# Kernel tuning notes

Measured on AMD Instinct MI355X. Metric: run time of the kernel, lower is better.

The kernel has to match this reference:

```python
import jax, jax.numpy as jnp
import numpy as np

N_NODES = 10000
LN_EPS = 1e-5


def _gcn(x, W, b, src, dst):
    # GraphConvolution: linear transform then sum-aggregate messages over edges.
    sup = x @ W                               # [B, N, H]
    msg = sup[:, src, :]                      # [B, E, H] gather from source nodes
    agg = jax.vmap(lambda m: jax.ops.segment_sum(m, dst, num_segments=N_NODES))(msg)
    return agg + b


def _layernorm(x, g, b):
    mu = jnp.mean(x, axis=-1, keepdims=True)
    var = jnp.var(x, axis=-1, keepdims=True)
    return (x - mu) * jax.lax.rsqrt(var + LN_EPS) * g + b


def _attention_pool(x, W, u, num_iterations=3):
    # x: [B, N, d] -> r: [B, 1, d]
    a = jnp.tanh(x @ W) @ u                   # [B, N]
    alpha = jax.nn.softmax(a, axis=1)
    r = jnp.einsum('bn,bnd->bd', alpha, x)
    for _ in range(num_iterations):
        beta = jax.nn.softmax(jnp.einsum('bnd,bd->bn', x, r), axis=1)
        r = jnp.einsum('bn,bnd->bd', beta, x)
    return r[:, None, :]


def _forward(x, src, dst, W_conv0, b_conv0, W_convs, b_convs,
             mW1, mb1, mW2, mb2, mW3, mb3,
             ln1_g, ln1_b, ln2_g, ln2_b, attnW, attnu, fW1, fb1, fW2, fb2,
             fcW, fcb):
    gelu = lambda t: jax.nn.gelu(t, approximate=False)
    # stacked GCN layers (first layer distinct input dim)
    x = gelu(_gcn(x, W_conv0, b_conv0, src, dst))
    for i in range(W_convs.shape[0]):
        x = gelu(_gcn(x, W_convs[i], b_convs[i], src, dst))
    # dropout is identity in eval mode
    # MLP head
    x = jax.nn.relu(x @ mW1 + mb1)
    x = jax.nn.relu(x @ mW2 + mb2)
    x = x @ mW3 + mb3
    # Encoder: 2 layers of (attention-pool residual + LN + FFN residual + LN)
    for i in range(2):
        x = x + _attention_pool(x, attnW[i], attnu[i])   # broadcast [B,1,d]
        x = _layernorm(x, ln1_g[i], ln1_b[i])
        h = jax.nn.relu(x @ fW1[i] + fb1[i]) @ fW2[i] + fb2[i]
        x = _layernorm(x + h, ln2_g[i], ln2_b[i])
    x = x @ fcW + fcb                          # [B, N, out]
    return x.mean(axis=1)                      # [B, out]


def setup_inputs() -> dict:
    key = jax.random.key(0)
    ks = jax.random.split(key, 32)
    B, N, E = 4, N_NODES, 160000
    F_in, H, D, A, OUT = 128, 256, 256, 8, 10
    s = lambda k, *shape: jax.random.normal(k, shape, jnp.float32) * 0.05
    return {
        'x': jax.random.normal(ks[0], (B, N, F_in), jnp.float32),
        'src': jax.random.randint(ks[1], (E,), 0, N, jnp.int32),
        'dst': jax.random.randint(ks[2], (E,), 0, N, jnp.int32),
        'W_conv0': s(ks[3], F_in, H), 'b_conv0': s(ks[4], H),
        'W_convs': s(ks[5], 3, H, H), 'b_convs': s(ks[6], 3, H),
        'mW1': s(ks[7], H, H // 2), 'mb1': s(ks[8], H // 2),
        'mW2': s(ks[9], H // 2, H // 4), 'mb2': s(ks[10], H // 4),
        'mW3': s(ks[11], H // 4, D), 'mb3': s(ks[12], D),
        'ln1_g': jnp.ones((2, D), jnp.float32), 'ln1_b': jnp.zeros((2, D), jnp.float32),
        'ln2_g': jnp.ones((2, D), jnp.float32), 'ln2_b': jnp.zeros((2, D), jnp.float32),
        'attnW': s(ks[13], 2, D, A), 'attnu': s(ks[14], 2, A),
        'fW1': s(ks[15], 2, D, H), 'fb1': s(ks[16], 2, H),
        'fW2': s(ks[17], 2, H, D), 'fb2': s(ks[18], 2, D),
        'fcW': s(ks[19], D, OUT), 'fcb': s(ks[20], OUT),
    }


def reference(x, src, dst, W_conv0, b_conv0, W_convs, b_convs,
              mW1, mb1, mW2, mb2, mW3, mb3,
              ln1_g, ln1_b, ln2_g, ln2_b, attnW, attnu, fW1, fb1, fW2, fb2,
              fcW, fcb):
    return _forward(x, src, dst, W_conv0, b_conv0, W_convs, b_convs,
                    mW1, mb1, mW2, mb2, mW3, mb3,
                    ln1_g, ln1_b, ln2_g, ln2_b, attnW, attnu, fW1, fb1, fW2, fb2,
                    fcW, fcb)
```

## Files before the change

### kernel.cpp

```cpp
#include <hip/hip_runtime.h>
#include <math.h>

#define NN 10000
#define NB 4
#define NE 160000
#define DM 256
#define MR (NB * NN)
#define LN_EPS 1e-5f
#define PCH 40
#define NCH (NN / PCH)
#define CCH 100

typedef __attribute__((ext_vector_type(8))) short short8;
typedef __attribute__((ext_vector_type(4))) float floatx4;


__device__ inline float bf2f(unsigned short u) {
    unsigned int x = ((unsigned int)u) << 16;
    float f;
    __builtin_memcpy(&f, &x, 4);
    return f;
}

__device__ inline unsigned short f2bf(float f) {
    unsigned int x;
    __builtin_memcpy(&x, &f, 4);
    unsigned int r = x + 0x7FFFu + ((x >> 16) & 1u);
    return (unsigned short)(r >> 16);
}

__device__ inline float gelu_exact(float x) {
    return 0.5f * x * (1.0f + erff(x * 0.70710678118654752f));
}

__device__ inline float waveAllReduce(float v) {
#pragma unroll
    for (int off = 32; off > 0; off >>= 1) v += __shfl_xor(v, off, 64);
    return v;
}

__device__ inline float group16Reduce(float v) {
#pragma unroll
    for (int off = 8; off > 0; off >>= 1) v += __shfl_xor(v, off, 64);
    return v;
}

__device__ inline void gld16(const unsigned short* g, unsigned short* l) {
    __builtin_amdgcn_global_load_lds((const __attribute__((address_space(1))) void*)g,
                                     (__attribute__((address_space(3))) void*)l, 16, 0, 0);
}


__global__ void zero_i32_kernel(int* p, int n) {
    int i = blockIdx.x * 256 + threadIdx.x;
    if (i < n) p[i] = 0;
}

__global__ void cvt_bf16_kernel(const float* __restrict__ in, unsigned short* __restrict__ out, int n) {
    int i = blockIdx.x * 256 + threadIdx.x;
    if (i < n) out[i] = f2bf(in[i]);
}

struct TD { const float* src; unsigned short* dst; int K; int N; };
struct TDs { TD d[11]; };

__global__ void transpose_all_kernel(TDs tds) {
    TD t = tds.d[blockIdx.y];
    int idx = blockIdx.x * 256 + threadIdx.x;
    int total = t.K * t.N;
    if (idx < total) {
        int n = idx / t.K;
        int k = idx - n * t.K;
        t.dst[idx] = f2bf(t.src[(size_t)k * t.N + n]);
    }
}


__global__ void hist_kernel(const int* __restrict__ dst, int* __restrict__ counts, int e) {
    int i = blockIdx.x * 256 + threadIdx.x;
    if (i < e) atomicAdd(&counts[dst[i]], 1);
}

__global__ __launch_bounds__(256) void scan_kernel(const int* __restrict__ counts,
                                                   int* __restrict__ row_ptr,
                                                   int* __restrict__ fill_pos, int n) {
    __shared__ int sums[256];
    int tid = threadIdx.x;
    int chunk = (n + 255) / 256;
    int s0 = tid * chunk;
    int s1 = min(n, s0 + chunk);
    int local = 0;
    for (int i = s0; i < s1; i++) local += counts[i];
    sums[tid] = local;
    __syncthreads();
    for (int off = 1; off < 256; off <<= 1) {
        int v = (tid >= off) ? sums[tid - off] : 0;
        __syncthreads();
        sums[tid] += v;
        __syncthreads();
    }
    int base = (tid == 0) ? 0 : sums[tid - 1];
    for (int i = s0; i < s1; i++) {
        row_ptr[i] = base;
        fill_pos[i] = base;
        base += counts[i];
    }
    if (tid == 255) row_ptr[n] = sums[255];
}

__global__ void fill_kernel(const int* __restrict__ src, const int* __restrict__ dst,
                            int* __restrict__ fill_pos, int* __restrict__ csr_src, int e) {
    int i = blockIdx.x * 256 + threadIdx.x;
    if (i < e) {
        int p = atomicAdd(&fill_pos[dst[i]], 1);
        csr_src[p] = src[i];
    }
}


template <int BN, int CM, int K>
__global__ __launch_bounds__(256) void mfma_gemm_kernel(
    const unsigned short* __restrict__ A, const unsigned short* __restrict__ Bt,
    const float* __restrict__ bias, void* __restrict__ Cp, int N, int act) {
    constexpr int NBF = BN / 32;
    constexpr int NI = K / 32;
    __shared__ unsigned short AsL[2][4 * 64 * 8];
    __shared__ unsigned short BsL[2][(BN / 16) * 64 * 8];

    const int tid = threadIdx.x;
    const int w = tid >> 6, l = tid & 63;
    const int wm = w >> 1, wn = w & 1;
    const int bm0 = blockIdx.y * 64;
    const int bn0 = blockIdx.x * BN;
    const int lm = l & 15, lq = l >> 4;

    floatx4 acc[2][NBF];
#pragma unroll
    for (int mi = 0; mi < 2; mi++)
#pragma unroll
        for (int ni = 0; ni < NBF; ni++) acc[mi][ni] = (floatx4){0.f, 0.f, 0.f, 0.f};

    const int a_row = bm0 + (tid >> 6) * 16 + (l & 15);
    const int s_kc = (l >> 4) * 8;
    int b_rown[BN / 64], b_kc[BN / 64];
#pragma unroll
    for (int cc = 0; cc < BN / 64; cc++) {
        int c = tid + cc * 256;
        b_rown[cc] = bn0 + (c >> 6) * 16 + (c & 15);
        b_kc[cc] = ((c & 63) >> 4) * 8;
    }

    gld16(&A[(size_t)a_row * K + s_kc], &AsL[0][tid * 8]);
#pragma unroll
    for (int cc = 0; cc < BN / 64; cc++) {
        int c = tid + cc * 256;
        gld16(&Bt[(size_t)b_rown[cc] * K + b_kc[cc]], &BsL[0][c * 8]);
    }

#pragma unroll
    for (int i = 0; i < NI; i++) {
        const int buf = i & 1;
        __syncthreads();
        if (i + 1 < NI) {
            int k0 = (i + 1) * 32;
            gld16(&A[(size_t)a_row * K + k0 + s_kc], &AsL[buf ^ 1][tid * 8]);
#pragma unroll
            for (int cc = 0; cc < BN / 64; cc++) {
                int c = tid + cc * 256;
                gld16(&Bt[(size_t)b_rown[cc] * K + k0 + b_kc[cc]], &BsL[buf ^ 1][c * 8]);
            }
        }
        short8 af[2], bfv[NBF];
#pragma unroll
        for (int mi = 0; mi < 2; mi++) af[mi] = *(short8*)&AsL[buf][((wm * 2 + mi) * 64 + l) * 8];
#pragma unroll
        for (int ni = 0; ni < NBF; ni++) bfv[ni] = *(short8*)&BsL[buf][((wn * NBF + ni) * 64 + l) * 8];
#pragma unroll
        for (int mi = 0; mi < 2; mi++)
#pragma unroll
            for (int ni = 0; ni < NBF; ni++)
                acc[mi][ni] = __builtin_amdgcn_mfma_f32_16x16x32_bf16(af[mi], bfv[ni], acc[mi][ni], 0, 0, 0);
    }

#pragma unroll
    for (int ni = 0; ni < NBF; ni++) {
        int col = bn0 + (wn * NBF + ni) * 16 + lm;
        float bv = bias ? bias[col] : 0.0f;
#pragma unroll
        for (int mi = 0; mi < 2; mi++) {
            int row0 = bm0 + (wm * 2 + mi) * 16 + lq * 4;
#pragma unroll
            for (int r = 0; r < 4; r++) {
                int row = row0 + r;
                float v = acc[mi][ni][r] + bv;
                if (act == 1) v = fmaxf(v, 0.0f);
                if (CM == 0) {
                    ((float*)Cp)[(size_t)row * N + col] = v;
                } else if (CM == 1) {
                    ((unsigned short*)Cp)[(size_t)row * N + col] = f2bf(v);
                } else {
                    int bb = row / NN;
                    int nn = row - bb * NN;
                    ((unsigned short*)Cp)[(size_t)nn * (NB * DM) + bb * DM + col] = f2bf(v);
                }
            }
        }
    }
}


__global__ __launch_bounds__(256) void gemm_ln_kernel(
    const unsigned short* __restrict__ A,
    const unsigned short* __restrict__ Bt,
    const float* __restrict__ bias,
    const unsigned short* __restrict__ x1,
    const float* __restrict__ g, const float* __restrict__ bt,
    unsigned short* __restrict__ out16) {
    constexpr int K = 256, NBF = 8, NI = K / 32;
    __shared__ unsigned short AsL[2][4 * 64 * 8];
    __shared__ unsigned short BsL[2][16 * 64 * 8];
    __shared__ float rs[2][64], rq[2][64];

    const int tid = threadIdx.x;
    const int w = tid >> 6, l = tid & 63;
    const int wm = w >> 1, wn = w & 1;
    const int bm0 = blockIdx.x * 64;
    const int lm = l & 15, lq = l >> 4;

    floatx4 acc[2][NBF];
#pragma unroll
    for (int mi = 0; mi < 2; mi++)
#pragma unroll
        for (int ni = 0; ni < NBF; ni++) acc[mi][ni] = (floatx4){0.f, 0.f, 0.f, 0.f};

    const int a_row = bm0 + (tid >> 6) * 16 + (l & 15);
    const int s_kc = (l >> 4) * 8;
    int b_rown[4], b_kc[4];
#pragma unroll
    for (int cc = 0; cc < 4; cc++) {
        int c = tid + cc * 256;
        b_rown[cc] = (c >> 6) * 16 + (c & 15);
        b_kc[cc] = ((c & 63) >> 4) * 8;
    }

    gld16(&A[(size_t)a_row * K + s_kc], &AsL[0][tid * 8]);
#pragma unroll
    for (int cc = 0; cc < 4; cc++) {
        int c = tid + cc * 256;
        gld16(&Bt[(size_t)b_rown[cc] * K + b_kc[cc]], &BsL[0][c * 8]);
    }

#pragma unroll
    for (int i = 0; i < NI; i++) {
        const int buf = i & 1;
        __syncthreads();
        if (i + 1 < NI) {
            int k0 = (i + 1) * 32;
            gld16(&A[(size_t)a_row * K + k0 + s_kc], &AsL[buf ^ 1][tid * 8]);
#pragma unroll
            for (int cc = 0; cc < 4; cc++) {
                int c = tid + cc * 256;
                gld16(&Bt[(size_t)b_rown[cc] * K + k0 + b_kc[cc]], &BsL[buf ^ 1][c * 8]);
            }
        }
        short8 af[2], bfv[NBF];
#pragma unroll
        for (int mi = 0; mi < 2; mi++) af[mi] = *(short8*)&AsL[buf][((wm * 2 + mi) * 64 + l) * 8];
#pragma unroll
        for (int ni = 0; ni < NBF; ni++) bfv[ni] = *(short8*)&BsL[buf][((wn * NBF + ni) * 64 + l) * 8];
#pragma unroll
        for (int mi = 0; mi < 2; mi++)
#pragma unroll
            for (int ni = 0; ni < NBF; ni++)
                acc[mi][ni] = __builtin_amdgcn_mfma_f32_16x16x32_bf16(af[mi], bfv[ni], acc[mi][ni], 0, 0, 0);
    }

    float fb[NBF], gv[NBF], bv[NBF];
#pragma unroll
    for (int ni = 0; ni < NBF; ni++) {
        int col = (wn * NBF + ni) * 16 + lm;
        fb[ni] = bias[col];
        gv[ni] = g[col];
        bv[ni] = bt[col];
    }
    float psum[2][4], psq[2][4];
#pragma unroll
    for (int mi = 0; mi < 2; mi++)
#pragma unroll
        for (int r = 0; r < 4; r++) { psum[mi][r] = 0.f; psq[mi][r] = 0.f; }

#pragma unroll
    for (int mi = 0; mi < 2; mi++) {
        int row0 = bm0 + (wm * 2 + mi) * 16 + lq * 4;
#pragma unroll
        for (int r = 0; r < 4; r++) {
#pragma unroll
            for (int ni = 0; ni < NBF; ni++) {
                int col = (wn * NBF + ni) * 16 + lm;
                float y = bf2f(x1[(size_t)(row0 + r) * DM + col]) + acc[mi][ni][r] + fb[ni];
                acc[mi][ni][r] = y;
                psum[mi][r] += y;
                psq[mi][r] += y * y;
            }
        }
    }
#pragma unroll
    for (int mi = 0; mi < 2; mi++)
#pragma unroll
        for (int r = 0; r < 4; r++) {
            float s = group16Reduce(psum[mi][r]);
            float q = group16Reduce(psq[mi][r]);
            if (lm == 0) {
                int rl = (wm * 2 + mi) * 16 + lq * 4 + r;
                rs[wn][rl] = s;
                rq[wn][rl] = q;
            }
        }
    __syncthreads();
#pragma unroll
    for (int mi = 0; mi < 2; mi++) {
        int row0 = bm0 + (wm * 2 + mi) * 16 + lq * 4;
#pragma unroll
        for (int r = 0; r < 4; r++) {
            int rl = (wm * 2 + mi) * 16 + lq * 4 + r;
            float s = rs[0][rl] + rs[1][rl];
            float q = rq[0][rl] + rq[1][rl];
            float mean = s * (1.0f / 256.0f);
            float var = q * (1.0f / 256.0f) - mean * mean;
            float rstd = rsqrtf(var + LN_EPS);
#pragma unroll
            for (int ni = 0; ni < NBF; ni++) {
                int col = (wn * NBF + ni) * 16 + lm;
                out16[(size_t)(row0 + r) * DM + col] =
                    f2bf((acc[mi][ni][r] - mean) * rstd * gv[ni] + bv[ni]);
            }
        }
    }
}


__global__ __launch_bounds__(256) void agg_kernel(const unsigned short* __restrict__ sup,
                                                  const int* __restrict__ row_ptr,
                                                  const int* __restrict__ csr_src,
                                                  const float* __restrict__ bias,
                                                  unsigned short* __restrict__ out) {
    int n = blockIdx.x;
    int w = threadIdx.x >> 6, l = threadIdx.x & 63;
    int s = row_ptr[n], e = row_ptr[n + 1];
    const int off = w * DM + l * 4;
    float a0 = 0.f, a1 = 0.f, a2 = 0.f, a3 = 0.f;
    int j = s;
    for (; j + 8 <= e; j += 8) {
        int idx[8];
#pragma unroll
        for (int k = 0; k < 8; k++) idx[k] = csr_src[j + k];
        ushort4 v[8];
#pragma unroll
        for (int k = 0; k < 8; k++) v[k] = *(const ushort4*)&sup[(size_t)idx[k] * (NB * DM) + off];
#pragma unroll
        for (int k = 0; k < 8; k++) {
            a0 += bf2f(v[k].x); a1 += bf2f(v[k].y);
            a2 += bf2f(v[k].z); a3 += bf2f(v[k].w);
        }
    }
    for (; j < e; j++) {
        ushort4 v = *(const ushort4*)&sup[(size_t)csr_src[j] * (NB * DM) + off];
        a0 += bf2f(v.x); a1 += bf2f(v.y); a2 += bf2f(v.z); a3 += bf2f(v.w);
    }
    int d0 = l * 4;
    const float4 bv = *(const float4*)&bias[d0];
    ushort4 o;
    o.x = f2bf(gelu_exact(a0 + bv.x));
    o.y = f2bf(gelu_exact(a1 + bv.y));
    o.z = f2bf(gelu_exact(a2 + bv.z));
    o.w = f2bf(gelu_exact(a3 + bv.w));
    *(ushort4*)&out[((size_t)w * NN + n) * DM + d0] = o;
}


template <int MODE>
__global__ __launch_bounds__(256) void attn_pool_kernel(const unsigned short* __restrict__ x16,
                                                        const float* __restrict__ W,
                                                        const float* __restrict__ u,
                                                        const float* __restrict__ r_in,
                                                        float* __restrict__ pm,
                                                        float* __restrict__ pl,
                                                        float* __restrict__ pv) {
    int c = blockIdx.x, b = blockIdx.y;
    int tid = threadIdx.x, w = tid >> 6, l = tid & 63;
    float4 rv = {0, 0, 0, 0};
    float u0[8];
    if (MODE == 1) {
        rv = *(const float4*)&r_in[b * DM + l * 4];
    } else {
#pragma unroll
        for (int j = 0; j < 8; j++) u0[j] = u[j];
    }
    int n0 = c * PCH;
    float m = -INFINITY, L = 0.0f;
    float v0 = 0.f, v1 = 0.f, v2 = 0.f, v3 = 0.f;
    for (int n = n0 + w; n < n0 + PCH; n += 4) {
        ushort4 xb = *(const ushort4*)&x16[((size_t)b * NN + n) * DM + l * 4];
        float x0 = bf2f(xb.x), x1 = bf2f(xb.y), x2 = bf2f(xb.z), x3 = bf2f(xb.w);
        float s;
        if (MODE == 1) {
            s = x0 * rv.x + x1 * rv.y + x2 * rv.z + x3 * rv.w;
            s = waveAllReduce(s);
        } else {
            const float4* Wv = (const float4*)W;
            int d0 = l * 4;
            float xs[4] = {x0, x1, x2, x3};
            float t[8] = {0, 0, 0, 0, 0, 0, 0, 0};
#pragma unroll
            for (int dd = 0; dd < 4; dd++) {
                float4 w0 = Wv[(d0 + dd) * 2 + 0];
                float4 w1 = Wv[(d0 + dd) * 2 + 1];
                t[0] += xs[dd] * w0.x; t[1] += xs[dd] * w0.y; t[2] += xs[dd] * w0.z; t[3] += xs[dd] * w0.w;
                t[4] += xs[dd] * w1.x; t[5] += xs[dd] * w1.y; t[6] += xs[dd] * w1.z; t[7] += xs[dd] * w1.w;
            }
#pragma unroll
            for (int jj = 0; jj < 8; jj++) t[jj] = waveAllReduce(t[jj]);
            s = 0.f;
#pragma unroll
            for (int jj = 0; jj < 8; jj++) s += tanhf(t[jj]) * u0[jj];
        }
        if (s > m) {
            float sc = __expf(m - s);
            L *= sc; v0 *= sc; v1 *= sc; v2 *= sc; v3 *= sc;
            m = s;
        }
        float wgt = __expf(s - m);
        L += wgt;
        v0 += wgt * x0; v1 += wgt * x1; v2 += wgt * x2; v3 += wgt * x3;
    }
    __shared__ float sm[4], sl[4];
    __shared__ float sv[4][DM];
    if (l == 0) { sm[w] = m; sl[w] = L; }
    float4 vv = {v0, v1, v2, v3};
    *(float4*)&sv[w][l * 4] = vv;
    __syncthreads();
    int d = tid;
    float M = fmaxf(fmaxf(sm[0], sm[1]), fmaxf(sm[2], sm[3]));
    float e0 = __expf(sm[0] - M), e1 = __expf(sm[1] - M);
    float e2 = __expf(sm[2] - M), e3 = __expf(sm[3] - M);
    float Lt = e0 * sl[0] + e1 * sl[1] + e2 * sl[2] + e3 * sl[3];
    float vd = e0 * sv[0][d] + e1 * sv[1][d] + e2 * sv[2][d] + e3 * sv[3][d];
    pv[((size_t)b * NCH + c) * DM + d] = vd;
    if (d == 0) {
        pm[b * NCH + c] = M;
        pl[b * NCH + c] = Lt;
    }
}

__global__ __launch_bounds__(256) void attn_combine_kernel(const float* __restrict__ pm,
                                                           const float* __restrict__ pl,
                                                           const float* __restrict__ pv,
                                                           float* __restrict__ r) {
    int b = blockIdx.x, tid = threadIdx.x;
    __shared__ float red[256];
    __shared__ float se[NCH];
    float mv = -INFINITY;
    for (int c = tid; c < NCH; c += 256) mv = fmaxf(mv, pm[b * NCH + c]);
    red[tid] = mv;
    __syncthreads();
    for (int off = 128; off > 0; off >>= 1) {
        if (tid < off) red[tid] = fmaxf(red[tid], red[tid + off]);
        __syncthreads();
    }
    float M = red[0];
    __syncthreads();
    float lsum = 0.0f;
    for (int c = tid; c < NCH; c += 256) {
        float e = __expf(pm[b * NCH + c] - M);
        se[c] = e;
        lsum += e * pl[b * NCH + c];
    }
    red[tid] = lsum;
    __syncthreads();
    for (int off = 128; off > 0; off >>= 1) {
        if (tid < off) red[tid] += red[tid + off];
        __syncthreads();
    }
    float L = red[0];
    __syncthreads();
    float acc = 0.0f;
    for (int c = 0; c < NCH; c++) acc += se[c] * pv[((size_t)b * NCH + c) * DM + tid];
    r[b * DM + tid] = acc / L;
}


__global__ __launch_bounds__(256) void ln_bcast_kernel(const unsigned short* __restrict__ x16,
                                                       const float* __restrict__ r,
                                                       const float* __restrict__ g,
                                                       const float* __restrict__ bt,
                                                       unsigned short* __restrict__ out16) {
    int l = threadIdx.x & 63, w = threadIdx.x >> 6;
    int row = blockIdx.x * 4 + w;
    int b = row / NN;
    ushort4 xb = *(const ushort4*)&x16[(size_t)row * DM + l * 4];
    float4 rv = *(const float4*)(r + (size_t)b * DM + l * 4);
    float4 y;
    y.x = bf2f(xb.x) + rv.x; y.y = bf2f(xb.y) + rv.y;
    y.z = bf2f(xb.z) + rv.z; y.w = bf2f(xb.w) + rv.w;
    float s = y.x + y.y + y.z + y.w;
    float sq = y.x * y.x + y.y * y.y + y.z * y.z + y.w * y.w;
    s = waveAllReduce(s);
    sq = waveAllReduce(sq);
    float mean = s * (1.0f / 256.0f);
    float var = sq * (1.0f / 256.0f) - mean * mean;
    float rstd = rsqrtf(var + LN_EPS);
    float4 gv = *(const float4*)(g + l * 4);
    float4 bv = *(const float4*)(bt + l * 4);
    ushort4 o;
    o.x = f2bf((y.x - mean) * rstd * gv.x + bv.x);
    o.y = f2bf((y.y - mean) * rstd * gv.y + bv.y);
    o.z = f2bf((y.z - mean) * rstd * gv.z + bv.z);
    o.w = f2bf((y.w - mean) * rstd * gv.w + bv.w);
    *(ushort4*)&out16[(size_t)row * DM + l * 4] = o;
}


__global__ __launch_bounds__(256) void colsum_kernel(const unsigned short* __restrict__ x16,
                                                     float* __restrict__ pcol) {
    int b = blockIdx.y, c = blockIdx.x, d = threadIdx.x;
    int n0 = c * CCH, n1 = n0 + CCH;
    float acc = 0.0f;
    for (int n = n0; n < n1; n++) acc += bf2f(x16[((size_t)b * NN + n) * DM + d]);
    pcol[((size_t)b * (NN / CCH) + c) * DM + d] = acc;
}

__global__ __launch_bounds__(256) void final_kernel(const float* __restrict__ pcol,
                                                    const float* __restrict__ fcW,
                                                    const float* __restrict__ fcb,
                                                    float* __restrict__ out) {
    int b = blockIdx.x, d = threadIdx.x;
    __shared__ float sx[DM];
    float acc = 0.0f;
    for (int c = 0; c < NN / CCH; c++) acc += pcol[((size_t)b * (NN / CCH) + c) * DM + d];
    sx[d] = acc;
    __syncthreads();
    if (d < 10) {
        float o = 0.0f;
        for (int k = 0; k < DM; k++) o += sx[k] * fcW[k * 10 + d];
        out[b * 10 + d] = o * (1.0f / NN) + fcb[d];
    }
}


extern "C" void kernel_launch(void* const* d_in, const int* in_sizes, int n_in,
                              void* d_out, int out_size, void* d_ws, size_t ws_size,
                              hipStream_t stream) {
    const float* x_in    = (const float*)d_in[0];
    const int*   src     = (const int*)d_in[1];
    const int*   dst     = (const int*)d_in[2];
    const float* W_conv0 = (const float*)d_in[3];
    const float* b_conv0 = (const float*)d_in[4];
    const float* W_convs = (const float*)d_in[5];
    const float* b_convs = (const float*)d_in[6];
    const float* mW1 = (const float*)d_in[7];
    const float* mb1 = (const float*)d_in[8];
    const float* mW2 = (const float*)d_in[9];
    const float* mb2 = (const float*)d_in[10];
    const float* mW3 = (const float*)d_in[11];
    const float* mb3 = (const float*)d_in[12];
    const float* ln1_g = (const float*)d_in[13];
    const float* ln1_b = (const float*)d_in[14];
    const float* ln2_g = (const float*)d_in[15];
    const float* ln2_b = (const float*)d_in[16];
    const float* attnW = (const float*)d_in[17];
    const float* attnu = (const float*)d_in[18];
    const float* fW1 = (const float*)d_in[19];
    const float* fb1 = (const float*)d_in[20];
    const float* fW2 = (const float*)d_in[21];
    const float* fb2 = (const float*)d_in[22];
    const float* fcW = (const float*)d_in[23];
    const float* fcb = (const float*)d_in[24];
    float* out = (float*)d_out;

    char* p = (char*)d_ws;
    auto alloc = [&](size_t bytes) { char* q = p; p += (bytes + 255) & ~(size_t)255; return q; };
    unsigned short* sup16 = (unsigned short*)alloc((size_t)MR * DM * 2);
    unsigned short* act16 = (unsigned short*)alloc((size_t)MR * DM * 2);
    unsigned short* b16   = (unsigned short*)alloc((size_t)MR * DM * 2);
    unsigned short* t1    = (unsigned short*)alloc((size_t)MR * 128 * 2);
    unsigned short* t2    = (unsigned short*)alloc((size_t)MR * 64 * 2);
    unsigned short* wt    = (unsigned short*)alloc((size_t)548864 * 2);
    float* rbuf = (float*)alloc(NB * DM * 4);
    float* pm0  = (float*)alloc(NB * NCH * 4);
    float* pl0  = (float*)alloc(NB * NCH * 4);
    float* pv0  = (float*)alloc((size_t)NB * NCH * DM * 4);
    float* pcol = (float*)alloc((size_t)NB * (NN / CCH) * DM * 4);
    int* counts   = (int*)alloc(NN * 4);
    int* row_ptr  = (int*)alloc((NN + 1) * 4);
    int* fill_pos = (int*)alloc(NN * 4);
    int* csr_src  = (int*)alloc(NE * 4);

    unsigned short* Wt_conv0 = wt;
    unsigned short* Wt_convs = Wt_conv0 + 32768;
    unsigned short* mW1t = Wt_convs + 196608;
    unsigned short* mW2t = mW1t + 32768;
    unsigned short* mW3t = mW2t + 8192;
    unsigned short* fW1t = mW3t + 16384;
    unsigned short* fW2t = fW1t + 131072;

    const dim3 blk(256);

    zero_i32_kernel<<<(NN + 255) / 256, blk, 0, stream>>>(counts, NN);
    hist_kernel<<<(NE + 255) / 256, blk, 0, stream>>>(dst, counts, NE);
    scan_kernel<<<1, blk, 0, stream>>>(counts, row_ptr, fill_pos, NN);
    fill_kernel<<<(NE + 255) / 256, blk, 0, stream>>>(src, dst, fill_pos, csr_src, NE);

    TDs tds;
    tds.d[0]  = {W_conv0, Wt_conv0, 128, 256};
    tds.d[1]  = {W_convs + 0 * 65536, Wt_convs + 0 * 65536, 256, 256};
    tds.d[2]  = {W_convs + 1 * 65536, Wt_convs + 1 * 65536, 256, 256};
    tds.d[3]  = {W_convs + 2 * 65536, Wt_convs + 2 * 65536, 256, 256};
    tds.d[4]  = {mW1, mW1t, 256, 128};
    tds.d[5]  = {mW2, mW2t, 128, 64};
    tds.d[6]  = {mW3, mW3t, 64, 256};
    tds.d[7]  = {fW1 + 0 * 65536, fW1t + 0 * 65536, 256, 256};
    tds.d[8]  = {fW1 + 1 * 65536, fW1t + 1 * 65536, 256, 256};
    tds.d[9]  = {fW2 + 0 * 65536, fW2t + 0 * 65536, 256, 256};
    tds.d[10] = {fW2 + 1 * 65536, fW2t + 1 * 65536, 256, 256};
    transpose_all_kernel<<<dim3(256, 11), blk, 0, stream>>>(tds);

    cvt_bf16_kernel<<<(MR * 128 + 255) / 256, blk, 0, stream>>>(x_in, t1, MR * 128);

    mfma_gemm_kernel<128, 2, 128><<<dim3(2, MR / 64), blk, 0, stream>>>(t1, Wt_conv0, nullptr, sup16, 256, 0);
    agg_kernel<<<NN, blk, 0, stream>>>(sup16, row_ptr, csr_src, b_conv0, act16);
    for (int i = 0; i < 3; i++) {
        mfma_gemm_kernel<128, 2, 256><<<dim3(2, MR / 64), blk, 0, stream>>>(act16, Wt_convs + (size_t)i * 65536, nullptr, sup16, 256, 0);
        agg_kernel<<<NN, blk, 0, stream>>>(sup16, row_ptr, csr_src, b_convs + (size_t)i * 256, act16);
    }

    mfma_gemm_kernel<128, 1, 256><<<dim3(1, MR / 64), blk, 0, stream>>>(act16, mW1t, mb1, t1, 128, 1);
    mfma_gemm_kernel<64, 1, 128><<<dim3(1, MR / 64), blk, 0, stream>>>(t1, mW2t, mb2, t2, 64, 1);
    mfma_gemm_kernel<128, 1, 64><<<dim3(2, MR / 64), blk, 0, stream>>>(t2, mW3t, mb3, act16, 256, 0);

    const dim3 poolGrid(NCH, NB);
    for (int i = 0; i < 2; i++) {
        const float* Wp = attnW + (size_t)i * DM * 8;
        const float* up = attnu + (size_t)i * 8;
        attn_pool_kernel<0><<<poolGrid, blk, 0, stream>>>(act16, Wp, up, nullptr, pm0, pl0, pv0);
        attn_combine_kernel<<<NB, blk, 0, stream>>>(pm0, pl0, pv0, rbuf);
        for (int it = 0; it < 3; it++) {
            attn_pool_kernel<1><<<poolGrid, blk, 0, stream>>>(act16, nullptr, nullptr, rbuf, pm0, pl0, pv0);
            attn_combine_kernel<<<NB, blk, 0, stream>>>(pm0, pl0, pv0, rbuf);
        }
        ln_bcast_kernel<<<MR / 4, blk, 0, stream>>>(act16, rbuf, ln1_g + (size_t)i * DM,
                                                    ln1_b + (size_t)i * DM, b16);
        mfma_gemm_kernel<128, 1, 256><<<dim3(2, MR / 64), blk, 0, stream>>>(b16, fW1t + (size_t)i * 65536,
                                                                            fb1 + (size_t)i * DM, sup16, 256, 1);
        gemm_ln_kernel<<<MR / 64, blk, 0, stream>>>(sup16, fW2t + (size_t)i * 65536,
                                                    fb2 + (size_t)i * DM, b16,
                                                    ln2_g + (size_t)i * DM, ln2_b + (size_t)i * DM,
                                                    act16);
    }

    colsum_kernel<<<dim3(NN / CCH, NB), blk, 0, stream>>>(act16, pcol);
    final_kernel<<<NB, blk, 0, stream>>>(pcol, fcW, fcb, out);
}
```

Baseline: 770.8 us.

## Remap GCN aggregation to one node per wave and widen GEMM N tiles

The aggregation kernel now assigns each wave a distinct destination node and splits the batch-by-feature row of 1024 values into 8 slices of 128 across blocks. Each lane loads 2 bf16 values per edge instead of 4, and the grid grows to 2*NN blocks. Separately, several GEMMs switch from two 128-wide column blocks to one 256-wide block per row tile, so each block reuses the A tile across the full output width. The trade-offs are fewer GEMM blocks with more registers each, and a shorter 4-byte per-lane gather with possibly more load imbalance across waves that handle nodes of different degree.

```diff
diff --git a/kernel.cpp b/kernel.cpp
--- a/kernel.cpp
+++ b/kernel.cpp
@@ -344,37 +344,35 @@
                                                   const int* __restrict__ csr_src,
                                                   const float* __restrict__ bias,
                                                   unsigned short* __restrict__ out) {
-    int n = blockIdx.x;
+    int slice = blockIdx.x & 7;
+    int ngrp = blockIdx.x >> 3;
     int w = threadIdx.x >> 6, l = threadIdx.x & 63;
+    int n = ngrp * 4 + w;
     int s = row_ptr[n], e = row_ptr[n + 1];
-    const int off = w * DM + l * 4;
-    float a0 = 0.f, a1 = 0.f, a2 = 0.f, a3 = 0.f;
+    const int off = slice * 128 + l * 2;
+    float a0 = 0.f, a1 = 0.f;
     int j = s;
     for (; j + 8 <= e; j += 8) {
         int idx[8];
 #pragma unroll
         for (int k = 0; k < 8; k++) idx[k] = csr_src[j + k];
-        ushort4 v[8];
-#pragma unroll
-        for (int k = 0; k < 8; k++) v[k] = *(const ushort4*)&sup[(size_t)idx[k] * (NB * DM) + off];
-#pragma unroll
-        for (int k = 0; k < 8; k++) {
-            a0 += bf2f(v[k].x); a1 += bf2f(v[k].y);
-            a2 += bf2f(v[k].z); a3 += bf2f(v[k].w);
-        }
+        ushort2 v[8];
+#pragma unroll
+        for (int k = 0; k < 8; k++) v[k] = *(const ushort2*)&sup[(size_t)idx[k] * (NB * DM) + off];
+#pragma unroll
+        for (int k = 0; k < 8; k++) { a0 += bf2f(v[k].x); a1 += bf2f(v[k].y); }
     }
     for (; j < e; j++) {
-        ushort4 v = *(const ushort4*)&sup[(size_t)csr_src[j] * (NB * DM) + off];
-        a0 += bf2f(v.x); a1 += bf2f(v.y); a2 += bf2f(v.z); a3 += bf2f(v.w);
-    }
-    int d0 = l * 4;
-    const float4 bv = *(const float4*)&bias[d0];
-    ushort4 o;
-    o.x = f2bf(gelu_exact(a0 + bv.x));
-    o.y = f2bf(gelu_exact(a1 + bv.y));
-    o.z = f2bf(gelu_exact(a2 + bv.z));
-    o.w = f2bf(gelu_exact(a3 + bv.w));
-    *(ushort4*)&out[((size_t)w * NN + n) * DM + d0] = o;
+        ushort2 v = *(const ushort2*)&sup[(size_t)csr_src[j] * (NB * DM) + off];
+        a0 += bf2f(v.x); a1 += bf2f(v.y);
+    }
+    int b = off >> 8;
+    int d = off & 255;
+    float b0 = bias[d], b1 = bias[d + 1];
+    ushort2 o;
+    o.x = f2bf(gelu_exact(a0 + b0));
+    o.y = f2bf(gelu_exact(a1 + b1));
+    *(ushort2*)&out[((size_t)b * NN + n) * DM + d] = o;
 }
 
 
@@ -626,16 +624,16 @@
 
     cvt_bf16_kernel<<<(MR * 128 + 255) / 256, blk, 0, stream>>>(x_in, t1, MR * 128);
 
-    mfma_gemm_kernel<128, 2, 128><<<dim3(2, MR / 64), blk, 0, stream>>>(t1, Wt_conv0, nullptr, sup16, 256, 0);
-    agg_kernel<<<NN, blk, 0, stream>>>(sup16, row_ptr, csr_src, b_conv0, act16);
+    mfma_gemm_kernel<256, 2, 128><<<dim3(1, MR / 64), blk, 0, stream>>>(t1, Wt_conv0, nullptr, sup16, 256, 0);
+    agg_kernel<<<NN * 2, blk, 0, stream>>>(sup16, row_ptr, csr_src, b_conv0, act16);
     for (int i = 0; i < 3; i++) {
-        mfma_gemm_kernel<128, 2, 256><<<dim3(2, MR / 64), blk, 0, stream>>>(act16, Wt_convs + (size_t)i * 65536, nullptr, sup16, 256, 0);
-        agg_kernel<<<NN, blk, 0, stream>>>(sup16, row_ptr, csr_src, b_convs + (size_t)i * 256, act16);
+        mfma_gemm_kernel<256, 2, 256><<<dim3(1, MR / 64), blk, 0, stream>>>(act16, Wt_convs + (size_t)i * 65536, nullptr, sup16, 256, 0);
+        agg_kernel<<<NN * 2, blk, 0, stream>>>(sup16, row_ptr, csr_src, b_convs + (size_t)i * 256, act16);
     }
 
     mfma_gemm_kernel<128, 1, 256><<<dim3(1, MR / 64), blk, 0, stream>>>(act16, mW1t, mb1, t1, 128, 1);
     mfma_gemm_kernel<64, 1, 128><<<dim3(1, MR / 64), blk, 0, stream>>>(t1, mW2t, mb2, t2, 64, 1);
-    mfma_gemm_kernel<128, 1, 64><<<dim3(2, MR / 64), blk, 0, stream>>>(t2, mW3t, mb3, act16, 256, 0);
+    mfma_gemm_kernel<256, 1, 64><<<dim3(1, MR / 64), blk, 0, stream>>>(t2, mW3t, mb3, act16, 256, 0);
 
     const dim3 poolGrid(NCH, NB);
     for (int i = 0; i < 2; i++) {
@@ -649,7 +647,7 @@
         }
         ln_bcast_kernel<<<MR / 4, blk, 0, stream>>>(act16, rbuf, ln1_g + (size_t)i * DM,
                                                     ln1_b + (size_t)i * DM, b16);
-        mfma_gemm_kernel<128, 1, 256><<<dim3(2, MR / 64), blk, 0, stream>>>(b16, fW1t + (size_t)i * 65536,
+        mfma_gemm_kernel<256, 1, 256><<<dim3(1, MR / 64), blk, 0, stream>>>(b16, fW1t + (size_t)i * 65536,
                                                                             fb1 + (size_t)i * DM, sup16, 256, 1);
         gemm_ln_kernel<<<MR / 64, blk, 0, stream>>>(sup16, fW2t + (size_t)i * 65536,
                                                     fb2 + (size_t)i * DM, b16,
```

Result: no change. 776.8 us (+0.8%).
